# Performance work log

Measured on AMD Instinct MI355X. Metric: run time of the kernel, lower is better.

Reference implementation:

```python
import math
import jax, jax.numpy as jnp
import numpy as np

D_MODEL = 1024
N_HEADS = 16
HEAD_DIM = 64          # block_size
NUM_RULES = 64
RANK = 8               # proj_rank = round(sqrt(head_dim)); also router_rank
SHARED_RANK = 32       # round(sqrt(d_model))
NUM_BLOCKS = 16        # min(in,out)//block_size = 1024//64; total_block_dim == d_model
B, S = 4, 1024
ROPE_BASE = 10000.0


def setup_inputs() -> dict:
    key = jax.random.key(0)
    ks = iter(jax.random.split(key, 32))
    def nrm(shape, s=0.02):
        return jax.random.normal(next(ks), shape, dtype=jnp.float32) * s
    inp = {
        "x": jax.random.normal(next(ks), (B, S, D_MODEL), dtype=jnp.float32),
        "target_rule_ids": jax.random.randint(next(ks), (B, S), 0, NUM_RULES),
    }
    for p in ("q", "k", "v", "o"):
        inp[p + "_si"] = nrm((D_MODEL, SHARED_RANK))
        inp[p + "_so"] = nrm((SHARED_RANK, D_MODEL))
        inp[p + "_ri"] = nrm((NUM_RULES, HEAD_DIM, RANK))
        inp[p + "_ro"] = nrm((NUM_RULES, RANK, HEAD_DIM))
        inp[p + "_lg"] = nrm((NUM_RULES, NUM_BLOCKS), 1.0 / math.sqrt(NUM_BLOCKS))
    inp["router_q"] = nrm((NUM_RULES, RANK))
    inp["router_k"] = nrm((NUM_RULES, RANK))
    return inp


def _rule_proj(x, rules, si, so, ri, ro, lg):
    """RuleAwareProjection.forward_rules_batched, de-permuted.

    The torch code argsorts tokens by rule, zero-pads per-rule buckets, runs
    bmm per rule and scatters back; mathematically that equals a per-token
    gather of the rule's low-rank adapter, which is what we compute here.
    x: [N, D_MODEL], rules: [N] int.
    """
    base = (x @ si) @ so                                  # shared low-rank path
    xb = x.reshape(-1, NUM_BLOCKS, HEAD_DIM)              # [N, nb, bs]
    h = jnp.einsum('nbs,nsr->nbr', xb, ri[rules])         # [N, nb, rank]
    a = jnp.einsum('nbr,nrt->nbt', h, ro[rules])          # [N, nb, bs]
    # temperature = 1/sqrt(num_blocks) => logits / temperature = logits*sqrt(nb)
    sel = jax.nn.softmax(lg[rules] * math.sqrt(NUM_BLOCKS), axis=-1)
    return base + (a * sel[:, :, None]).reshape(-1, D_MODEL)


def _rope(q, k):
    # q, k: [B, H, S, D]; interleaved-pair rotation, start_pos = 0.
    S_, D = q.shape[2], q.shape[3]
    pos = jnp.arange(S_, dtype=jnp.float32)[:, None]
    div = jnp.exp(jnp.arange(0, D, 2, dtype=jnp.float32) * (-math.log(ROPE_BASE) / D))
    f = pos * div                                         # [S, D/2]
    sin, cos = jnp.sin(f), jnp.cos(f)
    def rot(t):
        t1, t2 = t[..., 0::2], t[..., 1::2]
        return jnp.stack([t1 * cos - t2 * sin, t2 * cos + t1 * sin], axis=-1).reshape(t.shape)
    return rot(q), rot(k)


def reference(x, target_rule_ids,
              q_si, q_so, q_ri, q_ro, q_lg,
              k_si, k_so, k_ri, k_ro, k_lg,
              v_si, v_so, v_ri, v_ro, v_lg,
              o_si, o_so, o_ri, o_ro, o_lg,
              router_q, router_k):
    B_, S_, C = x.shape
    flat_x = x.reshape(-1, C)
    rules = target_rule_ids.reshape(-1)

    q = _rule_proj(flat_x, rules, q_si, q_so, q_ri, q_ro, q_lg)
    k = _rule_proj(flat_x, rules, k_si, k_so, k_ri, k_ro, k_lg)
    v = _rule_proj(flat_x, rules, v_si, v_so, v_ri, v_ro, v_lg)
    q = q.reshape(B_, S_, N_HEADS, HEAD_DIM).transpose(0, 2, 1, 3)
    k = k.reshape(B_, S_, N_HEADS, HEAD_DIM).transpose(0, 2, 1, 3)
    v = v.reshape(B_, S_, N_HEADS, HEAD_DIM).transpose(0, 2, 1, 3)
    q, k = _rope(q, k)

    # rule-routing sparse mask: cosine affinity between token rule embeddings
    rq = router_q[target_rule_ids]                        # [B, S, rank]
    rk = router_k[target_rule_ids]
    rqn = rq / jnp.maximum(jnp.linalg.norm(rq, axis=-1, keepdims=True), 1e-12)
    rkn = rk / jnp.maximum(jnp.linalg.norm(rk, axis=-1, keepdims=True), 1e-12)
    tau = 1.0 / math.log(max(math.e, RANK))
    aff = jnp.einsum('bqr,bkr->bqk', rqn, rkn) / tau       # [B, S, S]
    causal = jnp.tril(jnp.ones((S_, S_), dtype=bool))
    masked = jnp.where(causal[None], aff, -jnp.inf)
    top_k = max(2, int(math.sqrt(S_)))
    if S_ > top_k:
        thr = jax.lax.top_k(masked, top_k)[0][..., -1:]
        rule_mask = (masked >= thr) & causal[None]
    else:
        rule_mask = jnp.broadcast_to(causal[None], masked.shape)

    scores = jnp.einsum('bhqd,bhkd->bhqk', q, k) / math.sqrt(HEAD_DIM)
    scores = jnp.where(rule_mask[:, None], scores, -jnp.inf)
    attn = jax.nn.softmax(scores, axis=-1)
    out = jnp.einsum('bhqk,bhkd->bhqd', attn, v)
    out = out.transpose(0, 2, 1, 3).reshape(-1, C)
    out = _rule_proj(out, rules, o_si, o_so, o_ri, o_ro, o_lg)
    return out.reshape(B_, S_, C)
```

## Files before the change

kernel.cpp:

```cpp
#include <hip/hip_runtime.h>
#include <hip/hip_bf16.h>
#include <hip/hip_fp16.h>

#define D_MODEL 1024
#define N_HEADS 16
#define HEAD_DIM 64
#define NUM_RULES 64
#define RANK 8
#define SHARED_RANK 32
#define NUM_BLOCKS_ 16
#define BB 4
#define SS 1024
#define NTOK (BB*SS)
#define NGRP (NTOK/8)
#define NGRP4 (NTOK/4)

typedef __attribute__((ext_vector_type(8))) short bf16x8;
typedef __attribute__((ext_vector_type(4))) float f32x4;

__device__ __forceinline__ float bf2f(unsigned short u) {
  unsigned int i = ((unsigned int)u) << 16;
  float f;
  __builtin_memcpy(&f, &i, 4);
  return f;
}
__device__ __forceinline__ unsigned short f2bf(float f) {
  __hip_bfloat16 h = __float2bfloat16(f);
  unsigned short u;
  __builtin_memcpy(&u, &h, 2);
  return u;
}
__device__ __forceinline__ unsigned short f2h(float f) {
  __half h = __float2half(f);
  unsigned short u;
  __builtin_memcpy(&u, &h, 2);
  return u;
}
__device__ __forceinline__ float h2f(unsigned short u) {
  __half h;
  __builtin_memcpy(&h, &u, 2);
  return __half2float(h);
}
template<bool BF>
__device__ __forceinline__ float ldw(const void* p, size_t i) {
  if (BF) return bf2f(((const unsigned short*)p)[i]);
  else    return ((const float*)p)[i];
}

__global__ void detect_kernel(const unsigned short* __restrict__ x, int* __restrict__ flag) {
  const int lane = threadIdx.x;
  int good = 0;
  for (int i = 0; i < 4; i++) {
    unsigned short u = x[lane*4 + i];
    int e = (u >> 7) & 0xFF;
    good += (e == 0 || (e >= 100 && e <= 145)) ? 1 : 0;
  }
  for (int off = 32; off; off >>= 1) good += __shfl_xor(good, off);
  if (lane == 0) flag[0] = (good >= 224) ? 1 : 0;
}

template<bool BF>
__device__ __forceinline__ void precompute_body(
    const void* rq, const void* rk,
    const void* qlg, const void* klg, const void* vlg, const void* olg,
    float* __restrict__ M, float* __restrict__ sel)
{
  __shared__ float rqn[64][8], rkn[64][8];
  const int tid = threadIdx.x;
  if (tid < 64) {
    float v[8]; float s = 0.f;
    for (int i = 0; i < 8; i++) { v[i] = ldw<BF>(rq, tid*8+i); s += v[i]*v[i]; }
    float inv = 1.0f / fmaxf(sqrtf(s), 1e-12f);
    for (int i = 0; i < 8; i++) rqn[tid][i] = v[i]*inv;
  } else if (tid < 128) {
    int r = tid - 64;
    float v[8]; float s = 0.f;
    for (int i = 0; i < 8; i++) { v[i] = ldw<BF>(rk, r*8+i); s += v[i]*v[i]; }
    float inv = 1.0f / fmaxf(sqrtf(s), 1e-12f);
    for (int i = 0; i < 8; i++) rkn[r][i] = v[i]*inv;
  }
  __syncthreads();
  const float LN8 = 2.0794415416798357f;
  for (int idx = tid; idx < 64*64; idx += 256) {
    int i = idx >> 6, j = idx & 63;
    float d = 0.f;
    for (int t = 0; t < 8; t++) d += rqn[i][t]*rkn[j][t];
    M[idx] = d * LN8;
  }
  const void* lgs[4] = {qlg, klg, vlg, olg};
  {
    int r = tid & 63;
    const void* lg = lgs[tid >> 6];
    float e[NUM_BLOCKS_]; float mx = -1e30f;
    for (int b = 0; b < NUM_BLOCKS_; b++) {
      e[b] = ldw<BF>(lg, r*NUM_BLOCKS_ + b) * 4.0f;
      mx = fmaxf(mx, e[b]);
    }
    float s = 0.f;
    for (int b = 0; b < NUM_BLOCKS_; b++) { e[b] = expf(e[b]-mx); s += e[b]; }
    float inv = 1.0f/s;
    for (int b = 0; b < NUM_BLOCKS_; b++) sel[tid*NUM_BLOCKS_+b] = e[b]*inv;
  }
}

__global__ void precompute_kernel(
    const void* rq, const void* rk,
    const void* qlg, const void* klg, const void* vlg, const void* olg,
    float* M, float* sel, const int* __restrict__ flag)
{
  if (*flag) precompute_body<true >(rq, rk, qlg, klg, vlg, olg, M, sel);
  else       precompute_body<false>(rq, rk, qlg, klg, vlg, olg, M, sel);
}

__global__ __launch_bounds__(128) void prep_wb_kernel(
    const float* __restrict__ qsi, const float* __restrict__ ksi,
    const float* __restrict__ vsi, const float* __restrict__ osi,
    unsigned short* __restrict__ wh, unsigned short* __restrict__ wl,
    const int* __restrict__ flag)
{
  if (*flag) return;
  const int kt = blockIdx.x, p = blockIdx.y;
  const int tid = threadIdx.x, nt = tid >> 6, lane = tid & 63;
  const float* si = (p==0)?qsi:((p==1)?ksi:((p==2)?vsi:osi));
  const int col = nt*16 + (lane & 15);
  const int k0 = kt*32 + (lane >> 4)*8;
  size_t base = ((((size_t)p*32 + kt)*2 + nt)*64 + lane)*8;
  unsigned short h8[8], l8[8];
  #pragma unroll
  for (int j = 0; j < 8; j++) {
    float f = si[(size_t)(k0 + j)*SHARED_RANK + col];
    unsigned short hu = f2bf(f);
    h8[j] = hu;
    l8[j] = f2bf(f - bf2f(hu));
  }
  #pragma unroll
  for (int j = 0; j < 8; j++) { wh[base + j] = h8[j]; wl[base + j] = l8[j]; }
}

template<int NPROJ>
__device__ __forceinline__ void tt_mfma_body(
    const float* __restrict__ xin,
    const unsigned short* __restrict__ wh, const unsigned short* __restrict__ wl,
    int p0, float* __restrict__ ttg)
{
  const int NT = NPROJ*2;
  const int tile = blockIdx.x;
  const int tid = threadIdx.x, lane = tid & 63, w = tid >> 6;
  const int kq = lane >> 4;
  __shared__ float red[4][64][25];

  f32x4 acc[NT];
  #pragma unroll
  for (int i = 0; i < NT; i++) acc[i] = (f32x4){0.f,0.f,0.f,0.f};

  const float* xrow = xin + (size_t)(tile*16 + (lane & 15))*D_MODEL + kq*8;
  #pragma unroll 2
  for (int s = 0; s < 8; s++) {
    const int kt = w*8 + s;
    float4 a0 = *(const float4*)(xrow + kt*32);
    float4 a1 = *(const float4*)(xrow + kt*32 + 4);
    float av[8] = {a0.x,a0.y,a0.z,a0.w,a1.x,a1.y,a1.z,a1.w};
    bf16x8 ah, al;
    #pragma unroll
    for (int j = 0; j < 8; j++) {
      unsigned short hu = f2bf(av[j]);
      ah[j] = (short)hu;
      al[j] = (short)f2bf(av[j] - bf2f(hu));
    }
    #pragma unroll
    for (int p = 0; p < NPROJ; p++) {
      #pragma unroll
      for (int nt = 0; nt < 2; nt++) {
        size_t bidx = ((((size_t)(p0+p)*32 + kt)*2 + nt)*64 + lane)*8;
        bf16x8 bh = *(const bf16x8*)(wh + bidx);
        bf16x8 bl = *(const bf16x8*)(wl + bidx);
        f32x4 c = acc[p*2+nt];
        c = __builtin_amdgcn_mfma_f32_16x16x32_bf16(ah, bh, c, 0, 0, 0);
        c = __builtin_amdgcn_mfma_f32_16x16x32_bf16(al, bh, c, 0, 0, 0);
        c = __builtin_amdgcn_mfma_f32_16x16x32_bf16(ah, bl, c, 0, 0, 0);
        acc[p*2+nt] = c;
      }
    }
  }
  #pragma unroll
  for (int i = 0; i < NT; i++) {
    red[w][lane][i*4+0] = acc[i][0]; red[w][lane][i*4+1] = acc[i][1];
    red[w][lane][i*4+2] = acc[i][2]; red[w][lane][i*4+3] = acc[i][3];
  }
  __syncthreads();
  if (w == 0) {
    const int tok0 = tile*16 + (lane >> 4)*4;
    #pragma unroll
    for (int i = 0; i < NT; i++) {
      const int ys = i >> 1, jj = (i & 1)*16 + (lane & 15);
      #pragma unroll
      for (int r = 0; r < 4; r++) {
        float sum = red[0][lane][i*4+r] + red[1][lane][i*4+r]
                  + red[2][lane][i*4+r] + red[3][lane][i*4+r];
        ttg[((size_t)ys*NTOK + tok0 + r)*32 + jj] = sum;
      }
    }
  }
}

__global__ __launch_bounds__(256) void A_tt_mfma3(
    const float* __restrict__ xin,
    const unsigned short* __restrict__ wh, const unsigned short* __restrict__ wl,
    float* __restrict__ ttg, const int* __restrict__ flag)
{
  if (*flag) return;
  tt_mfma_body<3>(xin, wh, wl, 0, ttg);
}

__global__ __launch_bounds__(256) void A_tt_mfma1(
    const float* __restrict__ xin,
    const unsigned short* __restrict__ wh, const unsigned short* __restrict__ wl,
    float* __restrict__ ttg, const int* __restrict__ flag)
{
  if (*flag) return;
  tt_mfma_body<1>(xin, wh, wl, 3, ttg);
}

template<int NP>
__device__ __forceinline__ void hh_body(
    const float* __restrict__ xin, const int* __restrict__ rules,
    const float* __restrict__ ri0, const float* __restrict__ ri1,
    const float* __restrict__ ri2, float* __restrict__ hhg)
{
  const int g = blockIdx.x, n0 = g*8, tid = threadIdx.x;
  const int t = tid >> 5, blk = (tid >> 1) & 15, r0 = (tid & 1)*4;
  const int n = n0 + t;
  const int rule = rules[n];
  const float* xb = xin + (size_t)n*D_MODEL + blk*64;
  const float* wb[3];
  wb[0] = ri0 + (size_t)rule*512 + r0;
  if (NP > 1) {
    wb[1] = ri1 + (size_t)rule*512 + r0;
    wb[2] = ri2 + (size_t)rule*512 + r0;
  }
  float a[NP][4];
  #pragma unroll
  for (int p = 0; p < NP; p++) { a[p][0]=0.f; a[p][1]=0.f; a[p][2]=0.f; a[p][3]=0.f; }
  #pragma unroll 4
  for (int k4 = 0; k4 < 16; k4++) {
    float4 xv = *(const float4*)(xb + k4*4);
    #pragma unroll
    for (int q = 0; q < 4; q++) {
      const int k = k4*4 + q;
      float xq = (q==0)?xv.x:((q==1)?xv.y:((q==2)?xv.z:xv.w));
      #pragma unroll
      for (int p = 0; p < NP; p++) {
        float4 wv = *(const float4*)(wb[p] + (size_t)k*8);
        a[p][0] += xq*wv.x; a[p][1] += xq*wv.y; a[p][2] += xq*wv.z; a[p][3] += xq*wv.w;
      }
    }
  }
  #pragma unroll
  for (int p = 0; p < NP; p++) {
    float4 hv; hv.x=a[p][0]; hv.y=a[p][1]; hv.z=a[p][2]; hv.w=a[p][3];
    *(float4*)&hhg[((size_t)p*NTOK + n)*128 + blk*8 + r0] = hv;
  }
}

__global__ __launch_bounds__(256) void A_hh3_f32(
    const float* __restrict__ xin, const int* __restrict__ rules,
    const float* __restrict__ qri, const float* __restrict__ kri,
    const float* __restrict__ vri, float* __restrict__ hhg,
    const int* __restrict__ flag)
{
  if (*flag) return;
  hh_body<3>(xin, rules, qri, kri, vri, hhg);
}

__global__ __launch_bounds__(256) void A_hh1_f32(
    const float* __restrict__ xin, const int* __restrict__ rules,
    const float* __restrict__ ori, float* __restrict__ hhg,
    const int* __restrict__ flag)
{
  if (*flag) return;
  hh_body<1>(xin, rules, ori, ori, ori, hhg);
}

template<bool IN_BF, bool W_BF>
__device__ __forceinline__ void stageA_body(
    const void* __restrict__ xin, const int* __restrict__ rules,
    const void* __restrict__ si, const void* __restrict__ ri,
    float* __restrict__ ttg, float* __restrict__ hhg, int yslot)
{
  const int g = blockIdx.x, n0 = g*8, tid = threadIdx.x;
  __shared__ float xs[8][D_MODEL];
  __shared__ float tpart[8][32][9];
  __shared__ int rl[8];

  #pragma unroll
  for (int t = 0; t < 8; t++) {
    float4 f;
    if (IN_BF) {
      ushort4 u = ((const ushort4*)((const unsigned short*)xin + (size_t)(n0+t)*D_MODEL))[tid];
      f.x = bf2f(u.x); f.y = bf2f(u.y); f.z = bf2f(u.z); f.w = bf2f(u.w);
    } else {
      f = ((const float4*)xin)[(size_t)(n0+t)*(D_MODEL/4) + tid];
    }
    *(float4*)&xs[t][tid*4] = f;
  }
  if (tid < 8) rl[tid] = rules[n0 + tid];
  __syncthreads();

  {
    const int c = tid >> 5, j = tid & 31;
    float p[8];
    #pragma unroll
    for (int t = 0; t < 8; t++) p[t] = 0.f;
    #pragma unroll 4
    for (int d4 = 0; d4 < 32; d4++) {
      const int d = c*128 + d4*4;
      float w0 = ldw<W_BF>(si, (size_t)(d+0)*SHARED_RANK + j);
      float w1 = ldw<W_BF>(si, (size_t)(d+1)*SHARED_RANK + j);
      float w2 = ldw<W_BF>(si, (size_t)(d+2)*SHARED_RANK + j);
      float w3 = ldw<W_BF>(si, (size_t)(d+3)*SHARED_RANK + j);
      #pragma unroll
      for (int t = 0; t < 8; t++) {
        float4 xv = *(const float4*)&xs[t][d];
        p[t] += xv.x*w0 + xv.y*w1 + xv.z*w2 + xv.w*w3;
      }
    }
    #pragma unroll
    for (int t = 0; t < 8; t++) tpart[c][j][t] = p[t];
  }
  __syncthreads();

  {
    const int t = tid >> 5, j = tid & 31;
    float s = 0.f;
    #pragma unroll
    for (int c = 0; c < 8; c++) s += tpart[c][j][t];
    ttg[((size_t)yslot*NTOK + n0 + t)*32 + j] = s;
  }
  {
    const int t = tid >> 5, blk = (tid >> 1) & 15, r0 = (tid & 1)*4;
    const int rule = rl[t];
    float a0=0.f, a1=0.f, a2=0.f, a3=0.f;
    #pragma unroll 4
    for (int k4 = 0; k4 < 16; k4++) {
      const int kk = ((k4 + blk) & 15) * 4;
      float4 xv = *(const float4*)&xs[t][blk*64 + kk];
      #pragma unroll
      for (int q = 0; q < 4; q++) {
        const int k = kk + q;
        float w0,w1,w2,w3;
        if (W_BF) {
          ushort4 u = *(const ushort4*)((const unsigned short*)ri + (size_t)rule*512 + (size_t)k*8 + r0);
          w0=bf2f(u.x); w1=bf2f(u.y); w2=bf2f(u.z); w3=bf2f(u.w);
        } else {
          float4 u = *(const float4*)((const float*)ri + (size_t)rule*512 + (size_t)k*8 + r0);
          w0=u.x; w1=u.y; w2=u.z; w3=u.w;
        }
        float xq = (q==0)?xv.x:((q==1)?xv.y:((q==2)?xv.z:xv.w));
        a0 += xq*w0; a1 += xq*w1; a2 += xq*w2; a3 += xq*w3;
      }
    }
    float4 hv; hv.x=a0; hv.y=a1; hv.z=a2; hv.w=a3;
    *(float4*)&hhg[((size_t)yslot*NTOK + n0 + t)*128 + blk*8 + r0] = hv;
  }
}

__global__ __launch_bounds__(256) void A_qkv_bf16(
    const void* x, const int* rules,
    const void* qsi, const void* qri, const void* ksi, const void* kri,
    const void* vsi, const void* vri,
    float* ttg, float* hhg, const int* __restrict__ flag)
{
  if (!*flag) return;
  const int y = blockIdx.y;
  const void* si = (y==0)?qsi:((y==1)?ksi:vsi);
  const void* ri = (y==0)?qri:((y==1)?kri:vri);
  stageA_body<true,true>(x, rules, si, ri, ttg, hhg, y);
}

__global__ __launch_bounds__(256) void A_o_bf16(
    const void* ain, const int* rules, const void* osi, const void* ori,
    float* ttg, float* hhg, const int* __restrict__ flag)
{
  if (!*flag) return;
  stageA_body<false,true>(ain, rules, osi, ori, ttg, hhg, 0);
}

template<bool W_BF>
__device__ __forceinline__ void stageB_body(
    const float* __restrict__ ttg, const float* __restrict__ hhg,
    const int* __restrict__ rules,
    const void* __restrict__ so, const void* __restrict__ ro,
    const float* __restrict__ sel, void* __restrict__ out,
    int yslot, int do_rope, int out_bf)
{
  const int blk4 = blockIdx.x;
  const int n0 = blk4*4, tid = threadIdx.x;
  __shared__ float tt_lds[32][5];
  __shared__ float hh_lds[4][132];
  __shared__ int rl[4];

  if (tid < 128) {
    const int j = tid >> 2, t4 = tid & 3;
    tt_lds[j][t4] = ttg[((size_t)yslot*NTOK + n0 + t4)*32 + j];
  } else if (tid < 256 && (tid - 128) < 128) {
    const int i = tid - 128;
    const int t4 = i >> 5, c = (i*4) & 127;
    float4 hv = *(const float4*)&hhg[((size_t)yslot*NTOK + n0 + t4)*128 + c];
    *(float4*)&hh_lds[t4][c] = hv;
  }
  if (tid < 4) rl[tid] = rules[n0 + tid];
  __syncthreads();

  const int ch0 = tid*4;
  float a0[4], a1[4], a2[4], a3[4];
  #pragma unroll
  for (int t = 0; t < 4; t++) { a0[t]=0.f; a1[t]=0.f; a2[t]=0.f; a3[t]=0.f; }

  #pragma unroll 4
  for (int j = 0; j < 32; j++) {
    float w0, w1, w2, w3;
    if (W_BF) {
      ushort4 u = *(const ushort4*)((const unsigned short*)so + (size_t)j*D_MODEL + ch0);
      w0=bf2f(u.x); w1=bf2f(u.y); w2=bf2f(u.z); w3=bf2f(u.w);
    } else {
      float4 u = *(const float4*)((const float*)so + (size_t)j*D_MODEL + ch0);
      w0=u.x; w1=u.y; w2=u.z; w3=u.w;
    }
    #pragma unroll
    for (int t = 0; t < 4; t++) {
      float tv = tt_lds[j][t];
      a0[t] += tv*w0; a1[t] += tv*w1; a2[t] += tv*w2; a3[t] += tv*w3;
    }
  }

  const int blk = ch0 >> 6, tc = ch0 & 63;
  float inv0 = 0.f, inv1 = 0.f;
  if (do_rope) {
    inv0 = expf(-(float)tc     * (9.210340371976184f/64.0f));
    inv1 = expf(-(float)(tc+2) * (9.210340371976184f/64.0f));
  }
  #pragma unroll 2
  for (int t = 0; t < 4; t++) {
    const int rule = rl[t];
    float b0=0.f, b1=0.f, b2=0.f, b3=0.f;
    #pragma unroll
    for (int r = 0; r < 8; r++) {
      float w0,w1,w2,w3;
      if (W_BF) {
        ushort4 u = *(const ushort4*)((const unsigned short*)ro + (size_t)rule*512 + r*64 + tc);
        w0=bf2f(u.x); w1=bf2f(u.y); w2=bf2f(u.z); w3=bf2f(u.w);
      } else {
        float4 u = *(const float4*)((const float*)ro + (size_t)rule*512 + r*64 + tc);
        w0=u.x; w1=u.y; w2=u.z; w3=u.w;
      }
      float hv = hh_lds[t][blk*8 + r];
      b0 += hv*w0; b1 += hv*w1; b2 += hv*w2; b3 += hv*w3;
    }
    float sb = sel[rule*NUM_BLOCKS_ + blk];
    float e0 = a0[t] + b0*sb, o0 = a1[t] + b1*sb;
    float e1 = a2[t] + b2*sb, o1 = a3[t] + b3*sb;
    const int n = n0 + t;
    if (do_rope) {
      float spos = (float)(n & (SS-1));
      float sn0, cs0, sn1, cs1;
      sincosf(spos*inv0, &sn0, &cs0);
      sincosf(spos*inv1, &sn1, &cs1);
      float u0 = e0*cs0 - o0*sn0; o0 = o0*cs0 + e0*sn0; e0 = u0;
      float u1 = e1*cs1 - o1*sn1; o1 = o1*cs1 + e1*sn1; e1 = u1;
    }
    if (out_bf) {
      ushort4 uv; uv.x=f2bf(e0); uv.y=f2bf(o0); uv.z=f2bf(e1); uv.w=f2bf(o1);
      *(ushort4*)((unsigned short*)out + (size_t)n*D_MODEL + ch0) = uv;
    } else {
      float4 fv; fv.x=e0; fv.y=o0; fv.z=e1; fv.w=o1;
      *(float4*)((float*)out + (size_t)n*D_MODEL + ch0) = fv;
    }
  }
}

__global__ __launch_bounds__(256) void B_qkv(
    const float* ttg, const float* hhg, const int* rules,
    const void* qso, const void* qro, const void* kso, const void* kro,
    const void* vso, const void* vro,
    const float* sel, float* qb, unsigned short* kb, unsigned short* vb,
    const int* __restrict__ flag)
{
  const int y = blockIdx.y;
  const void* so = (y==0)?qso:((y==1)?kso:vso);
  const void* ro = (y==0)?qro:((y==1)?kro:vro);
  void* out = (y==0)?(void*)qb:((y==1)?(void*)kb:(void*)vb);
  if (*flag)
    stageB_body<true >(ttg, hhg, rules, so, ro, sel + y*1024, out, y, (y<2)?1:0, (y>=1)?1:0);
  else
    stageB_body<false>(ttg, hhg, rules, so, ro, sel + y*1024, out, y, (y<2)?1:0, (y>=1)?1:0);
}

__global__ __launch_bounds__(256) void B_o(
    const float* ttg, const float* hhg, const int* rules,
    const void* oso, const void* oro, const float* sel, void* out,
    const int* __restrict__ flag)
{
  if (*flag) stageB_body<true >(ttg, hhg, rules, oso, oro, sel, out, 0, 0, 1);
  else       stageB_body<false>(ttg, hhg, rules, oso, oro, sel, out, 0, 0, 0);
}

__global__ __launch_bounds__(64) void mask_kernel(
    const int* __restrict__ rules, const float* __restrict__ M,
    unsigned long long* __restrict__ am, unsigned int* __restrict__ rp)
{
  const int bid = blockIdx.x;
  const int b = bid >> 10, qi = bid & 1023;
  const int lane = threadIdx.x;
  __shared__ int rrow[SS];
  __shared__ float val[64];
  __shared__ int cnth[64];
  for (int i = lane; i < SS/4; i += 64)
    ((int4*)rrow)[i] = ((const int4*)(rules + b*SS))[i];
  cnth[lane] = 0;
  __syncthreads();
  if (qi < 16 && lane < 16) {
    const int gg = lane >> 2, nt = lane & 3;
    unsigned v = 0;
    #pragma unroll
    for (int j = 0; j < 4; j++)
      v |= ((unsigned)rrow[qi*64 + nt*16 + gg*4 + j] & 0xffu) << (8*j);
    rp[b*256 + qi*16 + lane] = v;
  }
  for (int k = lane; k <= qi; k += 64) atomicAdd(&cnth[rrow[k]], 1);
  const int qrule = rrow[qi];
  const float myv = M[qrule*64 + lane];
  val[lane] = myv;
  __syncthreads();
  const int c = cnth[lane];
  int A = 0;
  for (int r = 0; r < 64; r++) {
    int cr = __shfl(c, r);
    A += (val[r] > myv) ? cr : 0;
  }
  unsigned long long allowed = __ballot(A < 32);
  if (lane == 0) am[bid] = allowed;
}

__global__ __launch_bounds__(256) void vtrans_kernel(
    const unsigned short* __restrict__ vb, unsigned short* __restrict__ vt)
{
  const int st = blockIdx.x, h = blockIdx.y, b = blockIdx.z;
  __shared__ unsigned short t[64][72];
  const int tid = threadIdx.x;
  #pragma unroll
  for (int it = 0; it < 2; it++) {
    int i = tid + it*256;
    int r = i >> 3, c8 = (i & 7)*8;
    uint4 v = *(const uint4*)(vb + ((size_t)(b*SS + st*64 + r)*D_MODEL + h*HEAD_DIM + c8));
    t[c8+0][r] = (unsigned short)(v.x & 0xffffu);
    t[c8+1][r] = (unsigned short)(v.x >> 16);
    t[c8+2][r] = (unsigned short)(v.y & 0xffffu);
    t[c8+3][r] = (unsigned short)(v.y >> 16);
    t[c8+4][r] = (unsigned short)(v.z & 0xffffu);
    t[c8+5][r] = (unsigned short)(v.z >> 16);
    t[c8+6][r] = (unsigned short)(v.w & 0xffffu);
    t[c8+7][r] = (unsigned short)(v.w >> 16);
  }
  __syncthreads();
  #pragma unroll
  for (int it = 0; it < 2; it++) {
    int i = tid + it*256;
    int d = i >> 3, c8 = i & 7;
    const unsigned short* src = &t[d][c8*8];
    uint2 r1, r2;
    r1.x = (unsigned)src[0] | ((unsigned)src[1] << 16);
    r1.y = (unsigned)src[2] | ((unsigned)src[3] << 16);
    r2.x = (unsigned)src[4] | ((unsigned)src[5] << 16);
    r2.y = (unsigned)src[6] | ((unsigned)src[7] << 16);
    const int base = (c8 >> 2)*32 + 4*((c8 >> 1) & 1);
    const int p1 = base + 8*((2*c8)   & 3);
    const int p2 = base + 8*((2*c8+1) & 3);
    unsigned short* dst = vt + ((size_t)(b*N_HEADS + h)*HEAD_DIM + d)*SS + st*64;
    *(uint2*)(dst + p1) = r1;
    *(uint2*)(dst + p2) = r2;
  }
}

__global__ __launch_bounds__(256, 4) void attn_mfma_kernel(
    const float* __restrict__ qb,
    const unsigned short* __restrict__ kb,
    const unsigned short* __restrict__ vtb,
    const unsigned int* __restrict__ rp,
    const unsigned long long* __restrict__ am,
    unsigned short* __restrict__ Obuf,
    float* __restrict__ mlbuf,
    float* outb)
{
  const int x = blockIdx.x, b = blockIdx.y, h = blockIdx.z;
  int qt, k0t, k1t, pidx;
  bool partial;
  if (x < 9) { qt = x; k0t = 0; k1t = qt; partial = false; pidx = 0; }
  else {
    const int j = x - 9, qti = j >> 1, s = j & 1;
    qt = 9 + qti; partial = true;
    pidx = ((b*N_HEADS + h)*7 + qti)*2 + s;
    if (s == 0) { k0t = 0; k1t = 7; } else { k0t = 8; k1t = qt; }
  }
  const int tid = threadIdx.x, lane = tid & 63, w = tid >> 6;
  const int g = lane >> 4, ql = lane & 15;
  __shared__ unsigned short Ks[64*64];
  __shared__ unsigned short Vs[64*64];

  const unsigned short* kbase = kb + (size_t)b*SS*D_MODEL + h*HEAD_DIM;
  const unsigned short* vbase = vtb + (size_t)(b*N_HEADS + h)*HEAD_DIM*SS;
  const unsigned int* rpb = rp + b*256;

  const int srow = tid >> 3;
  const int spos = tid & 7;
  const int sc0 = (srow*8      + (spos ^ (srow      & 7)))*8;
  const int sc1 = ((srow+32)*8 + (spos ^ ((srow+32) & 7)))*8;

  const int qa = qt*64 + w*16 + ql;
  bf16x8 qfrag[2];
  {
    const float* qrow = qb + (size_t)(b*SS + qa)*D_MODEL + h*HEAD_DIM + g*8;
    #pragma unroll
    for (int kc = 0; kc < 2; kc++) {
      float4 f0 = *(const float4*)(qrow + kc*32);
      float4 f1 = *(const float4*)(qrow + kc*32 + 4);
      bf16x8 qv;
      qv[0] = (short)f2bf(f0.x*0.125f); qv[1] = (short)f2bf(f0.y*0.125f);
      qv[2] = (short)f2bf(f0.z*0.125f); qv[3] = (short)f2bf(f0.w*0.125f);
      qv[4] = (short)f2bf(f1.x*0.125f); qv[5] = (short)f2bf(f1.y*0.125f);
      qv[6] = (short)f2bf(f1.z*0.125f); qv[7] = (short)f2bf(f1.w*0.125f);
      qfrag[kc] = qv;
    }
  }
  const uint2 mm = *(const uint2*)(am + (size_t)b*SS + qa);
  const unsigned aqlo = mm.x, aqhi = mm.y;

  f32x4 Oacc[4];
  #pragma unroll
  for (int nt = 0; nt < 4; nt++) Oacc[nt] = (f32x4){0.f,0.f,0.f,0.f};
  float lrun = 0.f;

  {
    const size_t koff0 = (size_t)k0t*64;
    uint4 k0 = *(const uint4*)(kbase + (koff0 + srow)*D_MODEL + spos*8);
    uint4 k1 = *(const uint4*)(kbase + (koff0 + srow + 32)*D_MODEL + spos*8);
    uint4 v0 = *(const uint4*)(vbase + (size_t)srow*SS + koff0 + spos*8);
    uint4 v1 = *(const uint4*)(vbase + (size_t)(srow+32)*SS + koff0 + spos*8);
    *(uint4*)&Ks[sc0] = k0; *(uint4*)&Ks[sc1] = k1;
    *(uint4*)&Vs[sc0] = v0; *(uint4*)&Vs[sc1] = v1;
  }
  __syncthreads();

  for (int kt = k0t; kt <= k1t; kt++) {
    const uint4 ru4 = *(const uint4*)(rpb + kt*16 + g*4);
    uint4 nk0, nk1, nv0, nv1;
    if (kt < k1t) {
      const size_t koff = (size_t)(kt + 1)*64;
      nk0 = *(const uint4*)(kbase + (koff + srow)*D_MODEL + spos*8);
      nk1 = *(const uint4*)(kbase + (koff + srow + 32)*D_MODEL + spos*8);
      nv0 = *(const uint4*)(vbase + (size_t)srow*SS + koff + spos*8);
      nv1 = *(const uint4*)(vbase + (size_t)(srow+32)*SS + koff + spos*8);
    }

    f32x4 Sacc[4];
    __builtin_amdgcn_s_setprio(1);
    #pragma unroll
    for (int nt = 0; nt < 4; nt++) {
      const int key = nt*16 + ql;
      f32x4 c = (f32x4){0.f,0.f,0.f,0.f};
      #pragma unroll
      for (int kcq = 0; kcq < 2; kcq++) {
        int off = (key*128 + kcq*64 + g*16) ^ ((key & 7) << 4);
        bf16x8 kf = *(const bf16x8*)((const char*)Ks + off);
        c = __builtin_amdgcn_mfma_f32_16x16x32_bf16(kf, qfrag[kcq], c, 0, 0, 0);
      }
      Sacc[nt] = c;
    }
    __builtin_amdgcn_s_setprio(0);

    const bool needc = (kt == qt);
    const unsigned ruarr[4] = {ru4.x, ru4.y, ru4.z, ru4.w};
    unsigned pk[4][2];
    #pragma unroll
    for (int nt = 0; nt < 4; nt++) {
      float p[4];
      #pragma unroll
      for (int r = 0; r < 4; r++) {
        const unsigned rr = (ruarr[nt] >> (8*r)) & 0xffu;
        const unsigned bits = (rr >= 32) ? aqhi : aqlo;
        bool ok = ((bits >> (rr & 31u)) & 1u) != 0u;
        if (needc) ok = ok && ((kt*64 + nt*16 + g*4 + r) <= qa);
        p[r] = __expf(ok ? Sacc[nt][r] : -3e38f);
        lrun += p[r];
      }
      pk[nt][0] = (unsigned)f2bf(p[0]) | ((unsigned)f2bf(p[1]) << 16);
      pk[nt][1] = (unsigned)f2bf(p[2]) | ((unsigned)f2bf(p[3]) << 16);
    }

    __builtin_amdgcn_s_setprio(1);
    #pragma unroll
    for (int kc = 0; kc < 2; kc++) {
      union { unsigned u[4]; bf16x8 v; } U;
      U.u[0] = pk[2*kc][0];   U.u[1] = pk[2*kc][1];
      U.u[2] = pk[2*kc+1][0]; U.u[3] = pk[2*kc+1][1];
      const bf16x8 pa = U.v;
      #pragma unroll
      for (int ntd = 0; ntd < 4; ntd++) {
        const int d = ntd*16 + ql;
        int boff = (d*128 + kc*64 + g*16) ^ ((d & 7) << 4);
        bf16x8 vf = *(const bf16x8*)((const char*)Vs + boff);
        Oacc[ntd] = __builtin_amdgcn_mfma_f32_16x16x32_bf16(pa, vf, Oacc[ntd], 0, 0, 0);
      }
    }
    __builtin_amdgcn_s_setprio(0);
    __syncthreads();
    if (kt < k1t) {
      *(uint4*)&Ks[sc0] = nk0; *(uint4*)&Ks[sc1] = nk1;
      *(uint4*)&Vs[sc0] = nv0; *(uint4*)&Vs[sc1] = nv1;
      __syncthreads();
    }
  }

  lrun += __shfl_xor(lrun, 16);
  lrun += __shfl_xor(lrun, 32);

  if (!partial) {
    float invl[4];
    #pragma unroll
    for (int r = 0; r < 4; r++) invl[r] = 1.0f / __shfl(lrun, g*4 + r);
    #pragma unroll
    for (int nt = 0; nt < 4; nt++) {
      #pragma unroll
      for (int r = 0; r < 4; r++) {
        outb[(size_t)(b*SS + qt*64 + w*16 + g*4 + r)*D_MODEL + h*HEAD_DIM + nt*16 + ql]
            = Oacc[nt][r]*invl[r];
      }
    }
  } else {
    unsigned short* ob = Obuf + (size_t)pidx*4096;
    #pragma unroll
    for (int nt = 0; nt < 4; nt++) {
      #pragma unroll
      for (int r = 0; r < 4; r++) {
        const int row = w*16 + g*4 + r;
        ob[row*64 + nt*16 + ql] = f2h(Oacc[nt][r]);
      }
    }
    if (lane < 16) mlbuf[(size_t)pidx*64 + w*16 + lane] = lrun;
  }
}

__global__ __launch_bounds__(256) void attn_combine(
    const unsigned short* __restrict__ Obuf, const float* __restrict__ mlbuf,
    float* __restrict__ outb)
{
  const int qti = blockIdx.x, b = blockIdx.y, h = blockIdx.z;
  const int qt = 9 + qti;
  const int p0 = ((b*N_HEADS + h)*7 + qti)*2;
  const int tid = threadIdx.x;
  const int row = tid >> 2, c0 = (tid & 3)*16;
  const float l0 = mlbuf[(size_t)p0*64 + row];
  const float l1 = mlbuf[(size_t)(p0+1)*64 + row];
  const float inv = 1.0f / (l0 + l1);
  const unsigned short* o0 = Obuf + (size_t)p0*4096 + row*64 + c0;
  const unsigned short* o1 = Obuf + (size_t)(p0+1)*4096 + row*64 + c0;
  float* dst = outb + (size_t)(b*SS + qt*64 + row)*D_MODEL + h*HEAD_DIM + c0;
  #pragma unroll
  for (int j = 0; j < 16; j += 4) {
    float4 fv;
    fv.x = (h2f(o0[j+0]) + h2f(o1[j+0]))*inv;
    fv.y = (h2f(o0[j+1]) + h2f(o1[j+1]))*inv;
    fv.z = (h2f(o0[j+2]) + h2f(o1[j+2]))*inv;
    fv.w = (h2f(o0[j+3]) + h2f(o1[j+3]))*inv;
    *(float4*)(dst + j) = fv;
  }
}

extern "C" void kernel_launch(void* const* d_in, const int* in_sizes, int n_in,
                              void* d_out, int out_size, void* d_ws, size_t ws_size,
                              hipStream_t stream) {
  (void)in_sizes; (void)n_in; (void)out_size; (void)ws_size;
  const void* x    = d_in[0];
  const int* rules = (const int*)d_in[1];
  const void* q_si = d_in[2];  const void* q_so = d_in[3];
  const void* q_ri = d_in[4];  const void* q_ro = d_in[5];  const void* q_lg = d_in[6];
  const void* k_si = d_in[7];  const void* k_so = d_in[8];
  const void* k_ri = d_in[9];  const void* k_ro = d_in[10]; const void* k_lg = d_in[11];
  const void* v_si = d_in[12]; const void* v_so = d_in[13];
  const void* v_ri = d_in[14]; const void* v_ro = d_in[15]; const void* v_lg = d_in[16];
  const void* o_si = d_in[17]; const void* o_so = d_in[18];
  const void* o_ri = d_in[19]; const void* o_ro = d_in[20]; const void* o_lg = d_in[21];
  const void* rq   = d_in[22]; const void* rk   = d_in[23];

  char* ws = (char*)d_ws;
  const size_t MB = 1024*1024;
  float*          qb    = (float*)(ws);
  unsigned short* kb    = (unsigned short*)(ws + 16*MB);
  unsigned short* vb    = (unsigned short*)(ws + 24*MB);
  unsigned short* vtb   = (unsigned short*)(ws + 32*MB);
  float*          ttg   = (float*)(ws + 40*MB);
  float*          hhg   = (float*)(ws + 42*MB);
  unsigned short* Obuf  = (unsigned short*)(ws + 40*MB);
  float*          mlbuf = (float*)(ws + 47*MB);
  unsigned long long* amask = (unsigned long long*)(ws + 48*MB);
  float*          Mt    = (float*)(ws + 49*MB + 16*1024);
  float*          selt  = (float*)(ws + 49*MB + 32*1024);
  int*            flag  = (int*)  (ws + 49*MB + 48*1024);
  unsigned int*   rp    = (unsigned int*)(ws + 49*MB + 52*1024);
  unsigned short* wpkh  = (unsigned short*)(ws + 49*MB + 64*1024);
  unsigned short* wpkl  = (unsigned short*)(ws + 49*MB + 64*1024 + 256*1024);

  detect_kernel<<<1, 64, 0, stream>>>((const unsigned short*)x, flag);
  precompute_kernel<<<1, 256, 0, stream>>>(rq, rk, q_lg, k_lg, v_lg, o_lg, Mt, selt, flag);
  mask_kernel<<<NTOK, 64, 0, stream>>>(rules, Mt, amask, rp);
  prep_wb_kernel<<<dim3(32, 4), 128, 0, stream>>>(
      (const float*)q_si, (const float*)k_si, (const float*)v_si, (const float*)o_si,
      wpkh, wpkl, flag);

  A_qkv_bf16<<<dim3(NGRP, 3), 256, 0, stream>>>(x, rules, q_si, q_ri, k_si, k_ri, v_si, v_ri, ttg, hhg, flag);
  A_tt_mfma3<<<256, 256, 0, stream>>>((const float*)x, wpkh, wpkl, ttg, flag);
  A_hh3_f32<<<NGRP, 256, 0, stream>>>((const float*)x, rules,
      (const float*)q_ri, (const float*)k_ri, (const float*)v_ri, hhg, flag);

  B_qkv<<<dim3(NGRP4, 3), 256, 0, stream>>>(ttg, hhg, rules, q_so, q_ro, k_so, k_ro, v_so, v_ro,
                                            selt, qb, kb, vb, flag);

  vtrans_kernel<<<dim3(16, 16, 4), 256, 0, stream>>>(vb, vtb);
  attn_mfma_kernel<<<dim3(23, BB, N_HEADS), 256, 0, stream>>>(qb, kb, vtb, rp, amask,
                                                              Obuf, mlbuf, qb);
  attn_combine<<<dim3(7, BB, N_HEADS), 256, 0, stream>>>(Obuf, mlbuf, qb);

  A_o_bf16<<<dim3(NGRP, 1), 256, 0, stream>>>(qb, rules, o_si, o_ri, ttg, hhg, flag);
  A_tt_mfma1<<<256, 256, 0, stream>>>(qb, wpkh, wpkl, ttg, flag);
  A_hh1_f32<<<NGRP, 256, 0, stream>>>(qb, rules, (const float*)o_ri, hhg, flag);
  B_o<<<NGRP4, 256, 0, stream>>>(ttg, hhg, rules, o_so, o_ro, selt + 3*1024, d_out, flag);
}
```

Baseline: 271.8 us.

## Merge detect into precompute, precompute RoPE table, unify bf16 path onto MFMA kernels

Folds the dtype-detection kernel into the precompute kernel, which removes one launch. Adds a kernel that precomputes a cos/sin RoPE table, so stage B reads it instead of calling sincosf per element. Removes the separate bf16 stage-A kernels and templates the MFMA and hh kernels on input and weight dtype so both paths share them. Fewer launches and no per-element transcendentals, at the cost of an extra table read and one more small kernel.

```diff
diff --git a/kernel.cpp b/kernel.cpp
--- a/kernel.cpp
+++ b/kernel.cpp
@@ -45,18 +45,6 @@
 __device__ __forceinline__ float ldw(const void* p, size_t i) {
   if (BF) return bf2f(((const unsigned short*)p)[i]);
   else    return ((const float*)p)[i];
-}
-
-__global__ void detect_kernel(const unsigned short* __restrict__ x, int* __restrict__ flag) {
-  const int lane = threadIdx.x;
-  int good = 0;
-  for (int i = 0; i < 4; i++) {
-    unsigned short u = x[lane*4 + i];
-    int e = (u >> 7) & 0xFF;
-    good += (e == 0 || (e >= 100 && e <= 145)) ? 1 : 0;
-  }
-  for (int off = 32; off; off >>= 1) good += __shfl_xor(good, off);
-  if (lane == 0) flag[0] = (good >= 224) ? 1 : 0;
 }
 
 template<bool BF>
@@ -103,32 +91,54 @@
   }
 }
 
-__global__ void precompute_kernel(
+__global__ void detect_precompute_kernel(
+    const unsigned short* __restrict__ x, int* __restrict__ flag,
     const void* rq, const void* rk,
     const void* qlg, const void* klg, const void* vlg, const void* olg,
-    float* M, float* sel, const int* __restrict__ flag)
-{
-  if (*flag) precompute_body<true >(rq, rk, qlg, klg, vlg, olg, M, sel);
-  else       precompute_body<false>(rq, rk, qlg, klg, vlg, olg, M, sel);
-}
-
-__global__ __launch_bounds__(128) void prep_wb_kernel(
-    const float* __restrict__ qsi, const float* __restrict__ ksi,
-    const float* __restrict__ vsi, const float* __restrict__ osi,
-    unsigned short* __restrict__ wh, unsigned short* __restrict__ wl,
-    const int* __restrict__ flag)
-{
-  if (*flag) return;
+    float* M, float* sel)
+{
+  __shared__ int fl;
+  const int tid = threadIdx.x;
+  if (tid < 64) {
+    int good = 0;
+    for (int i = 0; i < 4; i++) {
+      unsigned short u = x[tid*4 + i];
+      int e = (u >> 7) & 0xFF;
+      good += (e == 0 || (e >= 100 && e <= 145)) ? 1 : 0;
+    }
+    for (int off = 32; off; off >>= 1) good += __shfl_xor(good, off);
+    if (tid == 0) { int g = (good >= 224) ? 1 : 0; flag[0] = g; fl = g; }
+  }
+  __syncthreads();
+  if (fl) precompute_body<true >(rq, rk, qlg, klg, vlg, olg, M, sel);
+  else    precompute_body<false>(rq, rk, qlg, klg, vlg, olg, M, sel);
+}
+
+__global__ __launch_bounds__(256) void rope_tab_kernel(float* __restrict__ tab) {
+  const int idx = blockIdx.x*256 + threadIdx.x;
+  const int pos = idx >> 5, i0 = idx & 31;
+  float inv = expf(-(float)(2*i0) * (9.210340371976184f/64.0f));
+  float sn, cs;
+  sincosf((float)pos * inv, &sn, &cs);
+  tab[idx*2+0] = cs;
+  tab[idx*2+1] = sn;
+}
+
+template<bool BF>
+__device__ __forceinline__ void prep_wb_body(
+    const void* qsi, const void* ksi, const void* vsi, const void* osi,
+    unsigned short* __restrict__ wh, unsigned short* __restrict__ wl)
+{
   const int kt = blockIdx.x, p = blockIdx.y;
   const int tid = threadIdx.x, nt = tid >> 6, lane = tid & 63;
-  const float* si = (p==0)?qsi:((p==1)?ksi:((p==2)?vsi:osi));
+  const void* si = (p==0)?qsi:((p==1)?ksi:((p==2)?vsi:osi));
   const int col = nt*16 + (lane & 15);
   const int k0 = kt*32 + (lane >> 4)*8;
   size_t base = ((((size_t)p*32 + kt)*2 + nt)*64 + lane)*8;
   unsigned short h8[8], l8[8];
   #pragma unroll
   for (int j = 0; j < 8; j++) {
-    float f = si[(size_t)(k0 + j)*SHARED_RANK + col];
+    float f = ldw<BF>(si, (size_t)(k0 + j)*SHARED_RANK + col);
     unsigned short hu = f2bf(f);
     h8[j] = hu;
     l8[j] = f2bf(f - bf2f(hu));
@@ -137,9 +147,17 @@
   for (int j = 0; j < 8; j++) { wh[base + j] = h8[j]; wl[base + j] = l8[j]; }
 }
 
-template<int NPROJ>
+__global__ __launch_bounds__(128) void prep_wb_kernel(
+    const void* qsi, const void* ksi, const void* vsi, const void* osi,
+    unsigned short* wh, unsigned short* wl, const int* __restrict__ flag)
+{
+  if (*flag) prep_wb_body<true >(qsi, ksi, vsi, osi, wh, wl);
+  else       prep_wb_body<false>(qsi, ksi, vsi, osi, wh, wl);
+}
+
+template<bool IN_BF, int NPROJ>
 __device__ __forceinline__ void tt_mfma_body(
-    const float* __restrict__ xin,
+    const void* __restrict__ xin,
     const unsigned short* __restrict__ wh, const unsigned short* __restrict__ wl,
     int p0, float* __restrict__ ttg)
 {
@@ -153,13 +171,24 @@
   #pragma unroll
   for (int i = 0; i < NT; i++) acc[i] = (f32x4){0.f,0.f,0.f,0.f};
 
-  const float* xrow = xin + (size_t)(tile*16 + (lane & 15))*D_MODEL + kq*8;
+  const size_t rowoff = (size_t)(tile*16 + (lane & 15))*D_MODEL + kq*8;
   #pragma unroll 2
   for (int s = 0; s < 8; s++) {
     const int kt = w*8 + s;
-    float4 a0 = *(const float4*)(xrow + kt*32);
-    float4 a1 = *(const float4*)(xrow + kt*32 + 4);
-    float av[8] = {a0.x,a0.y,a0.z,a0.w,a1.x,a1.y,a1.z,a1.w};
+    float av[8];
+    if (IN_BF) {
+      const unsigned short* xr = (const unsigned short*)xin + rowoff + kt*32;
+      ushort4 u0 = *(const ushort4*)(xr);
+      ushort4 u1 = *(const ushort4*)(xr + 4);
+      av[0]=bf2f(u0.x); av[1]=bf2f(u0.y); av[2]=bf2f(u0.z); av[3]=bf2f(u0.w);
+      av[4]=bf2f(u1.x); av[5]=bf2f(u1.y); av[6]=bf2f(u1.z); av[7]=bf2f(u1.w);
+    } else {
+      const float* xr = (const float*)xin + rowoff + kt*32;
+      float4 a0 = *(const float4*)(xr);
+      float4 a1 = *(const float4*)(xr + 4);
+      av[0]=a0.x; av[1]=a0.y; av[2]=a0.z; av[3]=a0.w;
+      av[4]=a1.x; av[5]=a1.y; av[6]=a1.z; av[7]=a1.w;
+    }
     bf16x8 ah, al;
     #pragma unroll
     for (int j = 0; j < 8; j++) {
@@ -204,54 +233,65 @@
 }
 
 __global__ __launch_bounds__(256) void A_tt_mfma3(
-    const float* __restrict__ xin,
+    const void* __restrict__ xin,
     const unsigned short* __restrict__ wh, const unsigned short* __restrict__ wl,
     float* __restrict__ ttg, const int* __restrict__ flag)
 {
-  if (*flag) return;
-  tt_mfma_body<3>(xin, wh, wl, 0, ttg);
+  if (*flag) tt_mfma_body<true, 3>(xin, wh, wl, 0, ttg);
+  else       tt_mfma_body<false,3>(xin, wh, wl, 0, ttg);
 }
 
 __global__ __launch_bounds__(256) void A_tt_mfma1(
-    const float* __restrict__ xin,
+    const void* __restrict__ xin,
     const unsigned short* __restrict__ wh, const unsigned short* __restrict__ wl,
     float* __restrict__ ttg, const int* __restrict__ flag)
 {
-  if (*flag) return;
-  tt_mfma_body<1>(xin, wh, wl, 3, ttg);
-}
-
-template<int NP>
+  (void)flag;
+  tt_mfma_body<false,1>(xin, wh, wl, 3, ttg);
+}
+
+template<bool IN_BF, bool W_BF, int NP>
 __device__ __forceinline__ void hh_body(
-    const float* __restrict__ xin, const int* __restrict__ rules,
-    const float* __restrict__ ri0, const float* __restrict__ ri1,
-    const float* __restrict__ ri2, float* __restrict__ hhg)
+    const void* __restrict__ xin, const int* __restrict__ rules,
+    const void* __restrict__ ri0, const void* __restrict__ ri1,
+    const void* __restrict__ ri2, float* __restrict__ hhg)
 {
   const int g = blockIdx.x, n0 = g*8, tid = threadIdx.x;
   const int t = tid >> 5, blk = (tid >> 1) & 15, r0 = (tid & 1)*4;
   const int n = n0 + t;
   const int rule = rules[n];
-  const float* xb = xin + (size_t)n*D_MODEL + blk*64;
-  const float* wb[3];
-  wb[0] = ri0 + (size_t)rule*512 + r0;
-  if (NP > 1) {
-    wb[1] = ri1 + (size_t)rule*512 + r0;
-    wb[2] = ri2 + (size_t)rule*512 + r0;
-  }
+  const size_t xoff = (size_t)n*D_MODEL + blk*64;
+  const void* wb[3];
+  wb[0] = ri0;
+  if (NP > 1) { wb[1] = ri1; wb[2] = ri2; }
   float a[NP][4];
   #pragma unroll
   for (int p = 0; p < NP; p++) { a[p][0]=0.f; a[p][1]=0.f; a[p][2]=0.f; a[p][3]=0.f; }
   #pragma unroll 4
   for (int k4 = 0; k4 < 16; k4++) {
-    float4 xv = *(const float4*)(xb + k4*4);
+    float xv[4];
+    if (IN_BF) {
+      ushort4 u = *(const ushort4*)((const unsigned short*)xin + xoff + k4*4);
+      xv[0]=bf2f(u.x); xv[1]=bf2f(u.y); xv[2]=bf2f(u.z); xv[3]=bf2f(u.w);
+    } else {
+      float4 u = *(const float4*)((const float*)xin + xoff + k4*4);
+      xv[0]=u.x; xv[1]=u.y; xv[2]=u.z; xv[3]=u.w;
+    }
     #pragma unroll
     for (int q = 0; q < 4; q++) {
       const int k = k4*4 + q;
-      float xq = (q==0)?xv.x:((q==1)?xv.y:((q==2)?xv.z:xv.w));
+      const float xq = xv[q];
       #pragma unroll
       for (int p = 0; p < NP; p++) {
-        float4 wv = *(const float4*)(wb[p] + (size_t)k*8);
-        a[p][0] += xq*wv.x; a[p][1] += xq*wv.y; a[p][2] += xq*wv.z; a[p][3] += xq*wv.w;
+        float w0,w1,w2,w3;
+        if (W_BF) {
+          ushort4 u = *(const ushort4*)((const unsigned short*)wb[p] + (size_t)rule*512 + (size_t)k*8 + r0);
+          w0=bf2f(u.x); w1=bf2f(u.y); w2=bf2f(u.z); w3=bf2f(u.w);
+        } else {
+          float4 u = *(const float4*)((const float*)wb[p] + (size_t)rule*512 + (size_t)k*8 + r0);
+          w0=u.x; w1=u.y; w2=u.z; w3=u.w;
+        }
+        a[p][0] += xq*w0; a[p][1] += xq*w1; a[p][2] += xq*w2; a[p][3] += xq*w3;
       }
     }
   }
@@ -262,127 +302,23 @@
   }
 }
 
-__global__ __launch_bounds__(256) void A_hh3_f32(
-    const float* __restrict__ xin, const int* __restrict__ rules,
-    const float* __restrict__ qri, const float* __restrict__ kri,
-    const float* __restrict__ vri, float* __restrict__ hhg,
+__global__ __launch_bounds__(256) void A_hh3(
+    const void* __restrict__ xin, const int* __restrict__ rules,
+    const void* __restrict__ qri, const void* __restrict__ kri,
+    const void* __restrict__ vri, float* __restrict__ hhg,
     const int* __restrict__ flag)
 {
-  if (*flag) return;
-  hh_body<3>(xin, rules, qri, kri, vri, hhg);
-}
-
-__global__ __launch_bounds__(256) void A_hh1_f32(
-    const float* __restrict__ xin, const int* __restrict__ rules,
-    const float* __restrict__ ori, float* __restrict__ hhg,
+  if (*flag) hh_body<true, true, 3>(xin, rules, qri, kri, vri, hhg);
+  else       hh_body<false,false,3>(xin, rules, qri, kri, vri, hhg);
+}
+
+__global__ __launch_bounds__(256) void A_hh1(
+    const void* __restrict__ xin, const int* __restrict__ rules,
+    const void* __restrict__ ori, float* __restrict__ hhg,
     const int* __restrict__ flag)
 {
-  if (*flag) return;
-  hh_body<1>(xin, rules, ori, ori, ori, hhg);
-}
-
-template<bool IN_BF, bool W_BF>
-__device__ __forceinline__ void stageA_body(
-    const void* __restrict__ xin, const int* __restrict__ rules,
-    const void* __restrict__ si, const void* __restrict__ ri,
-    float* __restrict__ ttg, float* __restrict__ hhg, int yslot)
-{
-  const int g = blockIdx.x, n0 = g*8, tid = threadIdx.x;
-  __shared__ float xs[8][D_MODEL];
-  __shared__ float tpart[8][32][9];
-  __shared__ int rl[8];
-
-  #pragma unroll
-  for (int t = 0; t < 8; t++) {
-    float4 f;
-    if (IN_BF) {
-      ushort4 u = ((const ushort4*)((const unsigned short*)xin + (size_t)(n0+t)*D_MODEL))[tid];
-      f.x = bf2f(u.x); f.y = bf2f(u.y); f.z = bf2f(u.z); f.w = bf2f(u.w);
-    } else {
-      f = ((const float4*)xin)[(size_t)(n0+t)*(D_MODEL/4) + tid];
-    }
-    *(float4*)&xs[t][tid*4] = f;
-  }
-  if (tid < 8) rl[tid] = rules[n0 + tid];
-  __syncthreads();
-
-  {
-    const int c = tid >> 5, j = tid & 31;
-    float p[8];
-    #pragma unroll
-    for (int t = 0; t < 8; t++) p[t] = 0.f;
-    #pragma unroll 4
-    for (int d4 = 0; d4 < 32; d4++) {
-      const int d = c*128 + d4*4;
-      float w0 = ldw<W_BF>(si, (size_t)(d+0)*SHARED_RANK + j);
-      float w1 = ldw<W_BF>(si, (size_t)(d+1)*SHARED_RANK + j);
-      float w2 = ldw<W_BF>(si, (size_t)(d+2)*SHARED_RANK + j);
-      float w3 = ldw<W_BF>(si, (size_t)(d+3)*SHARED_RANK + j);
-      #pragma unroll
-      for (int t = 0; t < 8; t++) {
-        float4 xv = *(const float4*)&xs[t][d];
-        p[t] += xv.x*w0 + xv.y*w1 + xv.z*w2 + xv.w*w3;
-      }
-    }
-    #pragma unroll
-    for (int t = 0; t < 8; t++) tpart[c][j][t] = p[t];
-  }
-  __syncthreads();
-
-  {
-    const int t = tid >> 5, j = tid & 31;
-    float s = 0.f;
-    #pragma unroll
-    for (int c = 0; c < 8; c++) s += tpart[c][j][t];
-    ttg[((size_t)yslot*NTOK + n0 + t)*32 + j] = s;
-  }
-  {
-    const int t = tid >> 5, blk = (tid >> 1) & 15, r0 = (tid & 1)*4;
-    const int rule = rl[t];
-    float a0=0.f, a1=0.f, a2=0.f, a3=0.f;
-    #pragma unroll 4
-    for (int k4 = 0; k4 < 16; k4++) {
-      const int kk = ((k4 + blk) & 15) * 4;
-      float4 xv = *(const float4*)&xs[t][blk*64 + kk];
-      #pragma unroll
-      for (int q = 0; q < 4; q++) {
-        const int k = kk + q;
-        float w0,w1,w2,w3;
-        if (W_BF) {
-          ushort4 u = *(const ushort4*)((const unsigned short*)ri + (size_t)rule*512 + (size_t)k*8 + r0);
-          w0=bf2f(u.x); w1=bf2f(u.y); w2=bf2f(u.z); w3=bf2f(u.w);
-        } else {
-          float4 u = *(const float4*)((const float*)ri + (size_t)rule*512 + (size_t)k*8 + r0);
-          w0=u.x; w1=u.y; w2=u.z; w3=u.w;
-        }
-        float xq = (q==0)?xv.x:((q==1)?xv.y:((q==2)?xv.z:xv.w));
-        a0 += xq*w0; a1 += xq*w1; a2 += xq*w2; a3 += xq*w3;
-      }
-    }
-    float4 hv; hv.x=a0; hv.y=a1; hv.z=a2; hv.w=a3;
-    *(float4*)&hhg[((size_t)yslot*NTOK + n0 + t)*128 + blk*8 + r0] = hv;
-  }
-}
-
-__global__ __launch_bounds__(256) void A_qkv_bf16(
-    const void* x, const int* rules,
-    const void* qsi, const void* qri, const void* ksi, const void* kri,
-    const void* vsi, const void* vri,
-    float* ttg, float* hhg, const int* __restrict__ flag)
-{
-  if (!*flag) return;
-  const int y = blockIdx.y;
-  const void* si = (y==0)?qsi:((y==1)?ksi:vsi);
-  const void* ri = (y==0)?qri:((y==1)?kri:vri);
-  stageA_body<true,true>(x, rules, si, ri, ttg, hhg, y);
-}
-
-__global__ __launch_bounds__(256) void A_o_bf16(
-    const void* ain, const int* rules, const void* osi, const void* ori,
-    float* ttg, float* hhg, const int* __restrict__ flag)
-{
-  if (!*flag) return;
-  stageA_body<false,true>(ain, rules, osi, ori, ttg, hhg, 0);
+  if (*flag) hh_body<false,true, 1>(xin, rules, ori, ori, ori, hhg);
+  else       hh_body<false,false,1>(xin, rules, ori, ori, ori, hhg);
 }
 
 template<bool W_BF>
@@ -390,7 +326,8 @@
     const float* __restrict__ ttg, const float* __restrict__ hhg,
     const int* __restrict__ rules,
     const void* __restrict__ so, const void* __restrict__ ro,
-    const float* __restrict__ sel, void* __restrict__ out,
+    const float* __restrict__ sel, const float* __restrict__ ropet,
+    void* __restrict__ out,
     int yslot, int do_rope, int out_bf)
 {
   const int blk4 = blockIdx.x;
@@ -434,11 +371,6 @@
   }
 
   const int blk = ch0 >> 6, tc = ch0 & 63;
-  float inv0 = 0.f, inv1 = 0.f;
-  if (do_rope) {
-    inv0 = expf(-(float)tc     * (9.210340371976184f/64.0f));
-    inv1 = expf(-(float)(tc+2) * (9.210340371976184f/64.0f));
-  }
   #pragma unroll 2
   for (int t = 0; t < 4; t++) {
     const int rule = rl[t];
@@ -461,12 +393,9 @@
     float e1 = a2[t] + b2*sb, o1 = a3[t] + b3*sb;
     const int n = n0 + t;
     if (do_rope) {
-      float spos = (float)(n & (SS-1));
-      float sn0, cs0, sn1, cs1;
-      sincosf(spos*inv0, &sn0, &cs0);
-      sincosf(spos*inv1, &sn1, &cs1);
-      float u0 = e0*cs0 - o0*sn0; o0 = o0*cs0 + e0*sn0; e0 = u0;
-      float u1 = e1*cs1 - o1*sn1; o1 = o1*cs1 + e1*sn1; e1 = u1;
+      float4 cs = *(const float4*)(ropet + ((size_t)(n & (SS-1))*32 + (tc >> 1))*2);
+      float u0 = e0*cs.x - o0*cs.y; o0 = o0*cs.x + e0*cs.y; e0 = u0;
+      float u1 = e1*cs.z - o1*cs.w; o1 = o1*cs.z + e1*cs.w; e1 = u1;
     }
     if (out_bf) {
       ushort4 uv; uv.x=f2bf(e0); uv.y=f2bf(o0); uv.z=f2bf(e1); uv.w=f2bf(o1);
@@ -482,7 +411,8 @@
     const float* ttg, const float* hhg, const int* rules,
     const void* qso, const void* qro, const void* kso, const void* kro,
     const void* vso, const void* vro,
-    const float* sel, float* qb, unsigned short* kb, unsigned short* vb,
+    const float* sel, const float* ropet,
+    float* qb, unsigned short* kb, unsigned short* vb,
     const int* __restrict__ flag)
 {
   const int y = blockIdx.y;
@@ -490,18 +420,18 @@
   const void* ro = (y==0)?qro:((y==1)?kro:vro);
   void* out = (y==0)?(void*)qb:((y==1)?(void*)kb:(void*)vb);
   if (*flag)
-    stageB_body<true >(ttg, hhg, rules, so, ro, sel + y*1024, out, y, (y<2)?1:0, (y>=1)?1:0);
+    stageB_body<true >(ttg, hhg, rules, so, ro, sel + y*1024, ropet, out, y, (y<2)?1:0, (y>=1)?1:0);
   else
-    stageB_body<false>(ttg, hhg, rules, so, ro, sel + y*1024, out, y, (y<2)?1:0, (y>=1)?1:0);
+    stageB_body<false>(ttg, hhg, rules, so, ro, sel + y*1024, ropet, out, y, (y<2)?1:0, (y>=1)?1:0);
 }
 
 __global__ __launch_bounds__(256) void B_o(
     const float* ttg, const float* hhg, const int* rules,
-    const void* oso, const void* oro, const float* sel, void* out,
-    const int* __restrict__ flag)
-{
-  if (*flag) stageB_body<true >(ttg, hhg, rules, oso, oro, sel, out, 0, 0, 1);
-  else       stageB_body<false>(ttg, hhg, rules, oso, oro, sel, out, 0, 0, 0);
+    const void* oso, const void* oro, const float* sel, const float* ropet,
+    void* out, const int* __restrict__ flag)
+{
+  if (*flag) stageB_body<true >(ttg, hhg, rules, oso, oro, sel, ropet, out, 0, 0, 1);
+  else       stageB_body<false>(ttg, hhg, rules, oso, oro, sel, ropet, out, 0, 0, 0);
 }
 
 __global__ __launch_bounds__(64) void mask_kernel(
@@ -808,29 +738,26 @@
   unsigned int*   rp    = (unsigned int*)(ws + 49*MB + 52*1024);
   unsigned short* wpkh  = (unsigned short*)(ws + 49*MB + 64*1024);
   unsigned short* wpkl  = (unsigned short*)(ws + 49*MB + 64*1024 + 256*1024);
-
-  detect_kernel<<<1, 64, 0, stream>>>((const unsigned short*)x, flag);
-  precompute_kernel<<<1, 256, 0, stream>>>(rq, rk, q_lg, k_lg, v_lg, o_lg, Mt, selt, flag);
+  float*          ropet = (float*)(ws + 50*MB);
+
+  detect_precompute_kernel<<<1, 256, 0, stream>>>(
+      (const unsigned short*)x, flag, rq, rk, q_lg, k_lg, v_lg, o_lg, Mt, selt);
   mask_kernel<<<NTOK, 64, 0, stream>>>(rules, Mt, amask, rp);
-  prep_wb_kernel<<<dim3(32, 4), 128, 0, stream>>>(
-      (const float*)q_si, (const float*)k_si, (const float*)v_si, (const float*)o_si,
-      wpkh, wpkl, flag);
-
-  A_qkv_bf16<<<dim3(NGRP, 3), 256, 0, stream>>>(x, rules, q_si, q_ri, k_si, k_ri, v_si, v_ri, ttg, hhg, flag);
-  A_tt_mfma3<<<256, 256, 0, stream>>>((const float*)x, wpkh, wpkl, ttg, flag);
-  A_hh3_f32<<<NGRP, 256, 0, stream>>>((const float*)x, rules,
-      (const float*)q_ri, (const float*)k_ri, (const float*)v_ri, hhg, flag);
+  rope_tab_kernel<<<128, 256, 0, stream>>>(ropet);
+  prep_wb_kernel<<<dim3(32, 4), 128, 0, stream>>>(q_si, k_si, v_si, o_si, wpkh, wpkl, flag);
+
+  A_tt_mfma3<<<256, 256, 0, stream>>>(x, wpkh, wpkl, ttg, flag);
+  A_hh3<<<NGRP, 256, 0, stream>>>(x, rules, q_ri, k_ri, v_ri, hhg, flag);
 
   B_qkv<<<dim3(NGRP4, 3), 256, 0, stream>>>(ttg, hhg, rules, q_so, q_ro, k_so, k_ro, v_so, v_ro,
-                                            selt, qb, kb, vb, flag);
+                                            selt, ropet, qb, kb, vb, flag);
 
   vtrans_kernel<<<dim3(16, 16, 4), 256, 0, stream>>>(vb, vtb);
   attn_mfma_kernel<<<dim3(23, BB, N_HEADS), 256, 0, stream>>>(qb, kb, vtb, rp, amask,
                                                               Obuf, mlbuf, qb);
   attn_combine<<<dim3(7, BB, N_HEADS), 256, 0, stream>>>(Obuf, mlbuf, qb);
 
-  A_o_bf16<<<dim3(NGRP, 1), 256, 0, stream>>>(qb, rules, o_si, o_ri, ttg, hhg, flag);
   A_tt_mfma1<<<256, 256, 0, stream>>>(qb, wpkh, wpkl, ttg, flag);
-  A_hh1_f32<<<NGRP, 256, 0, stream>>>(qb, rules, (const float*)o_ri, hhg, flag);
-  B_o<<<NGRP4, 256, 0, stream>>>(ttg, hhg, rules, o_so, o_ro, selt + 3*1024, d_out, flag);
-}
+  A_hh1<<<NGRP, 256, 0, stream>>>(qb, rules, o_ri, hhg, flag);
+  B_o<<<NGRP4, 256, 0, stream>>>(ttg, hhg, rules, o_so, o_ro, selt + 3*1024, ropet, d_out, flag);
+}
```

Result: faster. 257.0 us (-5.5%).
